# Performance work log

Measured on AMD Instinct MI355X. Metric: run time of the kernel, lower is better.

Reference implementation:

```python
import jax, jax.numpy as jnp
import numpy as np

LSTM_H = 4

def spp(x):
    # x: (N, C, H, W) -> (N, C*5) via adaptive max pool at levels [2, 1]
    N, C, H, W = x.shape
    p2 = x.reshape(N, C, 2, H // 2, 2, W // 2).max(axis=(3, 5)).reshape(N, C * 4)
    p1 = x.max(axis=(2, 3))  # (N, C)
    return jnp.concatenate([p2, p1], axis=1)  # (N, 15)

def setup_inputs() -> dict:
    key = jax.random.key(0)
    ks = jax.random.split(key, 12)
    B, S, C, H, W = 16, 128, 3, 224, 224
    s = 0.1
    return {
        "frames": jax.random.normal(ks[0], (B, S, C, H, W), dtype=jnp.float32),
        "Wf": jax.random.normal(ks[1], (15, 15), dtype=jnp.float32) * s,
        "bf": jax.random.normal(ks[2], (15,), dtype=jnp.float32) * s,
        "We": jax.random.normal(ks[3], (8, 15), dtype=jnp.float32) * s,
        "be": jax.random.normal(ks[4], (8,), dtype=jnp.float32) * s,
        "Wih": jax.random.normal(ks[5], (4 * LSTM_H, 8), dtype=jnp.float32) * s,
        "Whh": jax.random.normal(ks[6], (4 * LSTM_H, LSTM_H), dtype=jnp.float32) * s,
        "bih": jax.random.normal(ks[7], (4 * LSTM_H,), dtype=jnp.float32) * s,
        "bhh": jax.random.normal(ks[8], (4 * LSTM_H,), dtype=jnp.float32) * s,
        "Wp": jax.random.normal(ks[9], (1, LSTM_H), dtype=jnp.float32) * s,
        "bp": jax.random.normal(ks[10], (1,), dtype=jnp.float32) * s,
    }

def _lstm_cell(x, h, c, Wih, Whh, bih, bhh):
    gates = x @ Wih.T + h @ Whh.T + bih + bhh  # (B, 4H)
    i, f, g, o = jnp.split(gates, 4, axis=-1)  # torch gate order: i, f, g, o
    c2 = jax.nn.sigmoid(f) * c + jax.nn.sigmoid(i) * jnp.tanh(g)
    h2 = jax.nn.sigmoid(o) * jnp.tanh(c2)
    return h2, c2

def reference(frames, Wf, bf, We, be, Wih, Whh, bih, bhh, Wp, bp):
    B, S, C, H, W = frames.shape
    pooled_flat = spp(frames.reshape(B * S, C, H, W))          # (B*S, 15)
    forecasted_flat = pooled_flat @ Wf.T + bf                   # (B*S, 15)
    pooled = pooled_flat.reshape(B, S, 15)
    forecasted_pooled = forecasted_flat.reshape(B, S, 15)

    emb = pooled @ We.T + be                 # (B, S, 8)
    femb = forecasted_pooled @ We.T + be     # (B, S, 8)

    def step(carry, xs):
        h, c = carry
        e_t, fe_t = xs                       # each (B, 8)
        h1, c1 = _lstm_cell(e_t, h, c, Wih, Whh, bih, bhh)
        h2, _ = _lstm_cell(fe_t, h1, c1, Wih, Whh, bih, bhh)
        return (h1, c1), (h1, h2)

    h0 = jnp.zeros((B, LSTM_H), dtype=frames.dtype)
    c0 = jnp.zeros((B, LSTM_H), dtype=frames.dtype)
    xs = (jnp.swapaxes(emb, 0, 1), jnp.swapaxes(femb, 0, 1))   # (S, B, 8)
    _, (hs, fhs) = jax.lax.scan(step, (h0, c0), xs)            # (S, B, 4)

    progress = jax.nn.sigmoid(hs @ Wp.T + bp)[..., 0].T        # (B, S)
    forecasted_progress = jax.nn.sigmoid(fhs @ Wp.T + bp)[..., 0].T
    return (progress, forecasted_progress, pooled, forecasted_pooled)
```

## Files before the change

kernel.cpp:

```cpp
#include <hip/hip_runtime.h>
#include <math.h>

#define NEGINF (-INFINITY)

__global__ __launch_bounds__(256) void spp_kernel(const float* __restrict__ frames,
                                                  float* __restrict__ quad) {
    int cimg = blockIdx.x;
    const float4* __restrict__ base =
        reinterpret_cast<const float4*>(frames) + (size_t)cimg * 12544;
    int tid = threadIdx.x;
    float tl = NEGINF, tr = NEGINF, bl = NEGINF, br = NEGINF;
#pragma unroll 7
    for (int it = 0; it < 49; ++it) {
        int idx = (it << 8) + tid;
        float4 f = base[idx];
        float m = fmaxf(fmaxf(f.x, f.y), fmaxf(f.z, f.w));
        int row = idx / 56;
        int c4  = idx - row * 56;
        bool top  = row < 112;
        bool left = c4 < 28;
        float mt = top ? m : NEGINF;
        float mb = top ? NEGINF : m;
        tl = fmaxf(tl, left ? mt : NEGINF);
        tr = fmaxf(tr, left ? NEGINF : mt);
        bl = fmaxf(bl, left ? mb : NEGINF);
        br = fmaxf(br, left ? NEGINF : mb);
    }
#pragma unroll
    for (int m = 32; m >= 1; m >>= 1) {
        tl = fmaxf(tl, __shfl_xor(tl, m, 64));
        tr = fmaxf(tr, __shfl_xor(tr, m, 64));
        bl = fmaxf(bl, __shfl_xor(bl, m, 64));
        br = fmaxf(br, __shfl_xor(br, m, 64));
    }
    __shared__ float s[4][4];
    int w = tid >> 6;
    if ((tid & 63) == 0) { s[w][0] = tl; s[w][1] = tr; s[w][2] = bl; s[w][3] = br; }
    __syncthreads();
    if (tid < 4) {
        float r = fmaxf(fmaxf(s[0][tid], s[1][tid]), fmaxf(s[2][tid], s[3][tid]));
        quad[cimg * 4 + tid] = r;
    }
}

#define BSTRIDE 1036

template <int M>
__device__ __forceinline__ float qbcast(float v) {
    return __int_as_float(
        __builtin_amdgcn_update_dpp(0, __float_as_int(v), M * 0x55, 0xF, 0xF, true));
}

__device__ __forceinline__ float fsigmoid(float z) { return 1.f / (1.f + __expf(-z)); }
__device__ __forceinline__ float ftanh(float z) {
    z = fminf(fmaxf(z, -20.f), 20.f);
    float e = __expf(2.f * z);
    return (e - 1.f) / (e + 1.f);
}

__device__ __forceinline__ float dot8(const float4& a, const float4& b,
                                      const float* __restrict__ w) {
    return a.x * w[0] + a.y * w[1] + a.z * w[2] + a.w * w[3] +
           b.x * w[4] + b.y * w[5] + b.z * w[6] + b.w * w[7];
}

__global__ __launch_bounds__(512, 1) void prep_lstm_kernel(
    const float* __restrict__ quad, const float* __restrict__ Wf,
    const float* __restrict__ bf, const float* __restrict__ We,
    const float* __restrict__ be, const float* __restrict__ Wih,
    const float* __restrict__ Whh, const float* __restrict__ bih,
    const float* __restrict__ bhh, const float* __restrict__ Wp,
    const float* __restrict__ bp, float* __restrict__ out_pooled,
    float* __restrict__ out_fc, float* __restrict__ prog,
    float* __restrict__ fprog) {
    extern __shared__ float lds[];
    float* lemb  = lds;
    float* lfemb = lds + 16 * BSTRIDE;
    int tid = threadIdx.x;

    for (int n = tid; n < 2048; n += 512) {
        float p[15];
        float4 q0 = *(const float4*)(quad + n * 12);
        float4 q1 = *(const float4*)(quad + n * 12 + 4);
        float4 q2 = *(const float4*)(quad + n * 12 + 8);
        p[0] = q0.x; p[1] = q0.y; p[2] = q0.z; p[3] = q0.w;
        p[4] = q1.x; p[5] = q1.y; p[6] = q1.z; p[7] = q1.w;
        p[8] = q2.x; p[9] = q2.y; p[10] = q2.z; p[11] = q2.w;
#pragma unroll
        for (int c = 0; c < 3; c++)
            p[12 + c] = fmaxf(fmaxf(p[c * 4 + 0], p[c * 4 + 1]),
                              fmaxf(p[c * 4 + 2], p[c * 4 + 3]));
#pragma unroll
        for (int j = 0; j < 15; j++) out_pooled[n * 15 + j] = p[j];
        float fc[15];
#pragma unroll
        for (int j = 0; j < 15; j++) {
            float a = bf[j];
#pragma unroll
            for (int kk = 0; kk < 15; kk++) a += p[kk] * Wf[j * 15 + kk];
            fc[j] = a;
            out_fc[n * 15 + j] = a;
        }
        int b = n >> 7, sidx = n & 127;
        float* le = lemb  + b * BSTRIDE + sidx * 8;
        float* lf = lfemb + b * BSTRIDE + sidx * 8;
#pragma unroll
        for (int j = 0; j < 8; j++) {
            float a = be[j], a2 = be[j];
#pragma unroll
            for (int kk = 0; kk < 15; kk++) {
                a  += p[kk]  * We[j * 15 + kk];
                a2 += fc[kk] * We[j * 15 + kk];
            }
            le[j] = a;
            lf[j] = a2;
        }
    }
    __syncthreads();

    if (tid >= 64) return;
    int b = tid >> 2, k = tid & 3;
    float wih[4][8], whh[4][4], bsum[4];
#pragma unroll
    for (int g = 0; g < 4; g++) {
        int row = g * 4 + k;
#pragma unroll
        for (int m = 0; m < 8; m++) wih[g][m] = Wih[row * 8 + m];
#pragma unroll
        for (int m = 0; m < 4; m++) whh[g][m] = Whh[row * 4 + m];
        bsum[g] = bih[row] + bhh[row];
    }
    float wpv[4];
#pragma unroll
    for (int m = 0; m < 4; m++) wpv[m] = Wp[m];
    float bpv = bp[0];

    const float* xe = lemb  + b * BSTRIDE;
    const float* xf = lfemb + b * BSTRIDE;

    float xd1[4], xd2[4];
    {
        float4 a0 = *(const float4*)(xe);
        float4 a1 = *(const float4*)(xe + 4);
        float4 f0 = *(const float4*)(xf);
        float4 f1 = *(const float4*)(xf + 4);
#pragma unroll
        for (int g = 0; g < 4; g++) {
            xd1[g] = bsum[g] + dot8(a0, a1, wih[g]);
            xd2[g] = bsum[g] + dot8(f0, f1, wih[g]);
        }
    }

    float h0 = 0.f, h1r = 0.f, h2r = 0.f, h3r = 0.f;
    float ck = 0.f;

    for (int s2 = 0; s2 < 128; ++s2) {
        const float* nxe = xe + (s2 + 1) * 8;
        const float* nxf = xf + (s2 + 1) * 8;
        float4 na0 = *(const float4*)(nxe);
        float4 na1 = *(const float4*)(nxe + 4);
        float4 nf0 = *(const float4*)(nxf);
        float4 nf1 = *(const float4*)(nxf + 4);

        float g0 = xd1[0] + h0 * whh[0][0] + h1r * whh[0][1] + h2r * whh[0][2] + h3r * whh[0][3];
        float g1 = xd1[1] + h0 * whh[1][0] + h1r * whh[1][1] + h2r * whh[1][2] + h3r * whh[1][3];
        float g2 = xd1[2] + h0 * whh[2][0] + h1r * whh[2][1] + h2r * whh[2][2] + h3r * whh[2][3];
        float g3 = xd1[3] + h0 * whh[3][0] + h1r * whh[3][1] + h2r * whh[3][2] + h3r * whh[3][3];
        float c1  = fsigmoid(g1) * ck + fsigmoid(g0) * ftanh(g2);
        float hk1 = fsigmoid(g3) * ftanh(c1);
        float b0 = qbcast<0>(hk1), b1 = qbcast<1>(hk1), b2 = qbcast<2>(hk1), b3 = qbcast<3>(hk1);
        float z = bpv + b0 * wpv[0] + b1 * wpv[1] + b2 * wpv[2] + b3 * wpv[3];
        if (k == 0) prog[b * 128 + s2] = fsigmoid(z);

        float e0 = xd2[0] + b0 * whh[0][0] + b1 * whh[0][1] + b2 * whh[0][2] + b3 * whh[0][3];
        float e1 = xd2[1] + b0 * whh[1][0] + b1 * whh[1][1] + b2 * whh[1][2] + b3 * whh[1][3];
        float e2 = xd2[2] + b0 * whh[2][0] + b1 * whh[2][1] + b2 * whh[2][2] + b3 * whh[2][3];
        float e3 = xd2[3] + b0 * whh[3][0] + b1 * whh[3][1] + b2 * whh[3][2] + b3 * whh[3][3];
        float c2v = fsigmoid(e1) * c1 + fsigmoid(e0) * ftanh(e2);
        float hk2 = fsigmoid(e3) * ftanh(c2v);
        float d0 = qbcast<0>(hk2), d1 = qbcast<1>(hk2), d2 = qbcast<2>(hk2), d3 = qbcast<3>(hk2);
        float z2 = bpv + d0 * wpv[0] + d1 * wpv[1] + d2 * wpv[2] + d3 * wpv[3];
        if (k == 0) fprog[b * 128 + s2] = fsigmoid(z2);

        h0 = b0; h1r = b1; h2r = b2; h3r = b3; ck = c1;

#pragma unroll
        for (int g = 0; g < 4; g++) {
            xd1[g] = bsum[g] + dot8(na0, na1, wih[g]);
            xd2[g] = bsum[g] + dot8(nf0, nf1, wih[g]);
        }
    }
}

extern "C" void kernel_launch(void* const* d_in, const int* in_sizes, int n_in,
                              void* d_out, int out_size, void* d_ws, size_t ws_size,
                              hipStream_t stream) {
    const float* frames = (const float*)d_in[0];
    const float* Wf     = (const float*)d_in[1];
    const float* bf     = (const float*)d_in[2];
    const float* We     = (const float*)d_in[3];
    const float* be     = (const float*)d_in[4];
    const float* Wih    = (const float*)d_in[5];
    const float* Whh    = (const float*)d_in[6];
    const float* bih    = (const float*)d_in[7];
    const float* bhh    = (const float*)d_in[8];
    const float* Wp     = (const float*)d_in[9];
    const float* bp     = (const float*)d_in[10];

    float* out = (float*)d_out;
    float* out_prog   = out;
    float* out_fprog  = out + 2048;
    float* out_pooled = out + 4096;
    float* out_fc     = out + 4096 + 30720;

    float* quad = (float*)d_ws;

    spp_kernel<<<6144, 256, 0, stream>>>(frames, quad);
    size_t lds_bytes = (size_t)2 * 16 * BSTRIDE * sizeof(float);
    prep_lstm_kernel<<<1, 512, lds_bytes, stream>>>(quad, Wf, bf, We, be, Wih, Whh,
                                                    bih, bhh, Wp, bp, out_pooled,
                                                    out_fc, out_prog, out_fprog);
}
```

Before: 310.7 us.

## Fuse SPP and LSTM into one persistent kernel with per-timestep flag sync

The pooling kernel and the single-block prep/LSTM kernel become one launch of 257 blocks. Block 0 runs the LSTM recurrence and waits on per-timestep atomic counters, while 256 producer blocks pool frames in timestep order and write the embeddings to global memory. This lets the serial LSTM overlap the memory-bound pooling and removes the separate serial prep pass. In exchange, producers drop from 6144 blocks to 256, each handling a whole 3-channel image at a time. The design also relies on all blocks being co-resident to avoid deadlock, and it adds a memset launch.

```diff
diff --git a/kernel.cpp b/kernel.cpp
--- a/kernel.cpp
+++ b/kernel.cpp
@@ -2,55 +2,13 @@
 #include <math.h>
 
 #define NEGINF (-INFINITY)
-
-__global__ __launch_bounds__(256) void spp_kernel(const float* __restrict__ frames,
-                                                  float* __restrict__ quad) {
-    int cimg = blockIdx.x;
-    const float4* __restrict__ base =
-        reinterpret_cast<const float4*>(frames) + (size_t)cimg * 12544;
-    int tid = threadIdx.x;
-    float tl = NEGINF, tr = NEGINF, bl = NEGINF, br = NEGINF;
-#pragma unroll 7
-    for (int it = 0; it < 49; ++it) {
-        int idx = (it << 8) + tid;
-        float4 f = base[idx];
-        float m = fmaxf(fmaxf(f.x, f.y), fmaxf(f.z, f.w));
-        int row = idx / 56;
-        int c4  = idx - row * 56;
-        bool top  = row < 112;
-        bool left = c4 < 28;
-        float mt = top ? m : NEGINF;
-        float mb = top ? NEGINF : m;
-        tl = fmaxf(tl, left ? mt : NEGINF);
-        tr = fmaxf(tr, left ? NEGINF : mt);
-        bl = fmaxf(bl, left ? mb : NEGINF);
-        br = fmaxf(br, left ? NEGINF : mb);
-    }
-#pragma unroll
-    for (int m = 32; m >= 1; m >>= 1) {
-        tl = fmaxf(tl, __shfl_xor(tl, m, 64));
-        tr = fmaxf(tr, __shfl_xor(tr, m, 64));
-        bl = fmaxf(bl, __shfl_xor(bl, m, 64));
-        br = fmaxf(br, __shfl_xor(br, m, 64));
-    }
-    __shared__ float s[4][4];
-    int w = tid >> 6;
-    if ((tid & 63) == 0) { s[w][0] = tl; s[w][1] = tr; s[w][2] = bl; s[w][3] = br; }
-    __syncthreads();
-    if (tid < 4) {
-        float r = fmaxf(fmaxf(s[0][tid], s[1][tid]), fmaxf(s[2][tid], s[3][tid]));
-        quad[cimg * 4 + tid] = r;
-    }
-}
-
-#define BSTRIDE 1036
+#define AGENT __HIP_MEMORY_SCOPE_AGENT
 
 template <int M>
 __device__ __forceinline__ float qbcast(float v) {
     return __int_as_float(
         __builtin_amdgcn_update_dpp(0, __float_as_int(v), M * 0x55, 0xF, 0xF, true));
 }
-
 __device__ __forceinline__ float fsigmoid(float z) { return 1.f / (1.f + __expf(-z)); }
 __device__ __forceinline__ float ftanh(float z) {
     z = fminf(fmaxf(z, -20.f), 20.f);
@@ -58,65 +16,100 @@
     return (e - 1.f) / (e + 1.f);
 }
 
-__device__ __forceinline__ float dot8(const float4& a, const float4& b,
-                                      const float* __restrict__ w) {
-    return a.x * w[0] + a.y * w[1] + a.z * w[2] + a.w * w[3] +
-           b.x * w[4] + b.y * w[5] + b.z * w[6] + b.w * w[7];
-}
-
-__global__ __launch_bounds__(512, 1) void prep_lstm_kernel(
-    const float* __restrict__ quad, const float* __restrict__ Wf,
+__global__ __launch_bounds__(256) void fused_kernel(
+    const float* __restrict__ frames, const float* __restrict__ Wf,
     const float* __restrict__ bf, const float* __restrict__ We,
     const float* __restrict__ be, const float* __restrict__ Wih,
     const float* __restrict__ Whh, const float* __restrict__ bih,
     const float* __restrict__ bhh, const float* __restrict__ Wp,
     const float* __restrict__ bp, float* __restrict__ out_pooled,
     float* __restrict__ out_fc, float* __restrict__ prog,
-    float* __restrict__ fprog) {
-    extern __shared__ float lds[];
-    float* lemb  = lds;
-    float* lfemb = lds + 16 * BSTRIDE;
+    float* __restrict__ fprog, float* __restrict__ emb,
+    float* __restrict__ femb, int* __restrict__ cnt) {
     int tid = threadIdx.x;
 
-    for (int n = tid; n < 2048; n += 512) {
-        float p[15];
-        float4 q0 = *(const float4*)(quad + n * 12);
-        float4 q1 = *(const float4*)(quad + n * 12 + 4);
-        float4 q2 = *(const float4*)(quad + n * 12 + 8);
-        p[0] = q0.x; p[1] = q0.y; p[2] = q0.z; p[3] = q0.w;
-        p[4] = q1.x; p[5] = q1.y; p[6] = q1.z; p[7] = q1.w;
-        p[8] = q2.x; p[9] = q2.y; p[10] = q2.z; p[11] = q2.w;
-#pragma unroll
-        for (int c = 0; c < 3; c++)
-            p[12 + c] = fmaxf(fmaxf(p[c * 4 + 0], p[c * 4 + 1]),
-                              fmaxf(p[c * 4 + 2], p[c * 4 + 3]));
-#pragma unroll
-        for (int j = 0; j < 15; j++) out_pooled[n * 15 + j] = p[j];
-        float fc[15];
-#pragma unroll
-        for (int j = 0; j < 15; j++) {
-            float a = bf[j];
-#pragma unroll
-            for (int kk = 0; kk < 15; kk++) a += p[kk] * Wf[j * 15 + kk];
-            fc[j] = a;
-            out_fc[n * 15 + j] = a;
+    if (blockIdx.x > 0) {
+        int pid = blockIdx.x - 1;
+        __shared__ float sw[4][4];
+        __shared__ float sq[3][4];
+        __shared__ float sp[15];
+        __shared__ float sfc[15];
+        for (int r = 0; r < 8; ++r) {
+            int nidx = r * 256 + pid;
+            int s = nidx >> 4, b = nidx & 15;
+            int n = b * 128 + s;
+            const float4* __restrict__ base =
+                reinterpret_cast<const float4*>(frames) + (size_t)n * 37632;
+            for (int c = 0; c < 3; ++c) {
+                const float4* __restrict__ pb = base + c * 12544;
+                float tl = NEGINF, tr = NEGINF, bl = NEGINF, br = NEGINF;
+#pragma unroll 7
+                for (int it = 0; it < 49; ++it) {
+                    int i2 = (it << 8) + tid;
+                    float4 f = pb[i2];
+                    float m = fmaxf(fmaxf(f.x, f.y), fmaxf(f.z, f.w));
+                    int row = i2 / 56;
+                    int c4 = i2 - row * 56;
+                    bool top = row < 112;
+                    bool left = c4 < 28;
+                    float mt = top ? m : NEGINF;
+                    float mb = top ? NEGINF : m;
+                    tl = fmaxf(tl, left ? mt : NEGINF);
+                    tr = fmaxf(tr, left ? NEGINF : mt);
+                    bl = fmaxf(bl, left ? mb : NEGINF);
+                    br = fmaxf(br, left ? NEGINF : mb);
+                }
+#pragma unroll
+                for (int m = 32; m >= 1; m >>= 1) {
+                    tl = fmaxf(tl, __shfl_xor(tl, m, 64));
+                    tr = fmaxf(tr, __shfl_xor(tr, m, 64));
+                    bl = fmaxf(bl, __shfl_xor(bl, m, 64));
+                    br = fmaxf(br, __shfl_xor(br, m, 64));
+                }
+                int w = tid >> 6;
+                if ((tid & 63) == 0) { sw[w][0] = tl; sw[w][1] = tr; sw[w][2] = bl; sw[w][3] = br; }
+                __syncthreads();
+                if (tid < 4)
+                    sq[c][tid] = fmaxf(fmaxf(sw[0][tid], sw[1][tid]),
+                                       fmaxf(sw[2][tid], sw[3][tid]));
+                __syncthreads();
+            }
+            if (tid == 0) {
+#pragma unroll
+                for (int c = 0; c < 3; ++c) {
+                    float a = sq[c][0], bq = sq[c][1], cq = sq[c][2], d = sq[c][3];
+                    sp[c * 4 + 0] = a; sp[c * 4 + 1] = bq;
+                    sp[c * 4 + 2] = cq; sp[c * 4 + 3] = d;
+                    sp[12 + c] = fmaxf(fmaxf(a, bq), fmaxf(cq, d));
+                }
+            }
+            __syncthreads();
+            if (tid < 15) {
+                float a = bf[tid];
+#pragma unroll
+                for (int kk = 0; kk < 15; ++kk) a += sp[kk] * Wf[tid * 15 + kk];
+                sfc[tid] = a;
+                out_pooled[n * 15 + tid] = sp[tid];
+                out_fc[n * 15 + tid] = a;
+            }
+            __syncthreads();
+            if (tid < 8) {
+                float a = be[tid], a2 = be[tid];
+#pragma unroll
+                for (int kk = 0; kk < 15; ++kk) {
+                    a += sp[kk] * We[tid * 15 + kk];
+                    a2 += sfc[kk] * We[tid * 15 + kk];
+                }
+                __hip_atomic_store(&emb[n * 8 + tid], a, __ATOMIC_RELAXED, AGENT);
+                __hip_atomic_store(&femb[n * 8 + tid], a2, __ATOMIC_RELAXED, AGENT);
+            }
+            __syncthreads();
+            if (tid == 0)
+                __hip_atomic_fetch_add(&cnt[s], 1, __ATOMIC_RELEASE, AGENT);
+            __syncthreads();
         }
-        int b = n >> 7, sidx = n & 127;
-        float* le = lemb  + b * BSTRIDE + sidx * 8;
-        float* lf = lfemb + b * BSTRIDE + sidx * 8;
-#pragma unroll
-        for (int j = 0; j < 8; j++) {
-            float a = be[j], a2 = be[j];
-#pragma unroll
-            for (int kk = 0; kk < 15; kk++) {
-                a  += p[kk]  * We[j * 15 + kk];
-                a2 += fc[kk] * We[j * 15 + kk];
-            }
-            le[j] = a;
-            lf[j] = a2;
-        }
+        return;
     }
-    __syncthreads();
 
     if (tid >= 64) return;
     int b = tid >> 2, k = tid & 3;
@@ -135,42 +128,43 @@
     for (int m = 0; m < 4; m++) wpv[m] = Wp[m];
     float bpv = bp[0];
 
-    const float* xe = lemb  + b * BSTRIDE;
-    const float* xf = lfemb + b * BSTRIDE;
-
-    float xd1[4], xd2[4];
-    {
-        float4 a0 = *(const float4*)(xe);
-        float4 a1 = *(const float4*)(xe + 4);
-        float4 f0 = *(const float4*)(xf);
-        float4 f1 = *(const float4*)(xf + 4);
-#pragma unroll
-        for (int g = 0; g < 4; g++) {
-            xd1[g] = bsum[g] + dot8(a0, a1, wih[g]);
-            xd2[g] = bsum[g] + dot8(f0, f1, wih[g]);
-        }
-    }
-
     float h0 = 0.f, h1r = 0.f, h2r = 0.f, h3r = 0.f;
     float ck = 0.f;
 
-    for (int s2 = 0; s2 < 128; ++s2) {
-        const float* nxe = xe + (s2 + 1) * 8;
-        const float* nxf = xf + (s2 + 1) * 8;
-        float4 na0 = *(const float4*)(nxe);
-        float4 na1 = *(const float4*)(nxe + 4);
-        float4 nf0 = *(const float4*)(nxf);
-        float4 nf1 = *(const float4*)(nxf + 4);
+    for (int s = 0; s < 128; ++s) {
+        while (__hip_atomic_load(&cnt[s], __ATOMIC_ACQUIRE, AGENT) < 16) {
+            __builtin_amdgcn_s_sleep(1);
+        }
+        float* xe = emb + (size_t)(b * 128 + s) * 8;
+        float* xf = femb + (size_t)(b * 128 + s) * 8;
+        float x1[8], x2[8];
+#pragma unroll
+        for (int m = 0; m < 8; m++) x1[m] = __hip_atomic_load(&xe[m], __ATOMIC_RELAXED, AGENT);
+#pragma unroll
+        for (int m = 0; m < 8; m++) x2[m] = __hip_atomic_load(&xf[m], __ATOMIC_RELAXED, AGENT);
+
+        float xd1[4], xd2[4];
+#pragma unroll
+        for (int g = 0; g < 4; g++) {
+            float a = bsum[g], a2 = bsum[g];
+#pragma unroll
+            for (int m = 0; m < 8; m++) {
+                a += x1[m] * wih[g][m];
+                a2 += x2[m] * wih[g][m];
+            }
+            xd1[g] = a;
+            xd2[g] = a2;
+        }
 
         float g0 = xd1[0] + h0 * whh[0][0] + h1r * whh[0][1] + h2r * whh[0][2] + h3r * whh[0][3];
         float g1 = xd1[1] + h0 * whh[1][0] + h1r * whh[1][1] + h2r * whh[1][2] + h3r * whh[1][3];
         float g2 = xd1[2] + h0 * whh[2][0] + h1r * whh[2][1] + h2r * whh[2][2] + h3r * whh[2][3];
         float g3 = xd1[3] + h0 * whh[3][0] + h1r * whh[3][1] + h2r * whh[3][2] + h3r * whh[3][3];
-        float c1  = fsigmoid(g1) * ck + fsigmoid(g0) * ftanh(g2);
+        float c1 = fsigmoid(g1) * ck + fsigmoid(g0) * ftanh(g2);
         float hk1 = fsigmoid(g3) * ftanh(c1);
         float b0 = qbcast<0>(hk1), b1 = qbcast<1>(hk1), b2 = qbcast<2>(hk1), b3 = qbcast<3>(hk1);
         float z = bpv + b0 * wpv[0] + b1 * wpv[1] + b2 * wpv[2] + b3 * wpv[3];
-        if (k == 0) prog[b * 128 + s2] = fsigmoid(z);
+        if (k == 0) prog[b * 128 + s] = fsigmoid(z);
 
         float e0 = xd2[0] + b0 * whh[0][0] + b1 * whh[0][1] + b2 * whh[0][2] + b3 * whh[0][3];
         float e1 = xd2[1] + b0 * whh[1][0] + b1 * whh[1][1] + b2 * whh[1][2] + b3 * whh[1][3];
@@ -180,15 +174,9 @@
         float hk2 = fsigmoid(e3) * ftanh(c2v);
         float d0 = qbcast<0>(hk2), d1 = qbcast<1>(hk2), d2 = qbcast<2>(hk2), d3 = qbcast<3>(hk2);
         float z2 = bpv + d0 * wpv[0] + d1 * wpv[1] + d2 * wpv[2] + d3 * wpv[3];
-        if (k == 0) fprog[b * 128 + s2] = fsigmoid(z2);
+        if (k == 0) fprog[b * 128 + s] = fsigmoid(z2);
 
         h0 = b0; h1r = b1; h2r = b2; h3r = b3; ck = c1;
-
-#pragma unroll
-        for (int g = 0; g < 4; g++) {
-            xd1[g] = bsum[g] + dot8(na0, na1, wih[g]);
-            xd2[g] = bsum[g] + dot8(nf0, nf1, wih[g]);
-        }
     }
 }
 
@@ -213,11 +201,13 @@
     float* out_pooled = out + 4096;
     float* out_fc     = out + 4096 + 30720;
 
-    float* quad = (float*)d_ws;
-
-    spp_kernel<<<6144, 256, 0, stream>>>(frames, quad);
-    size_t lds_bytes = (size_t)2 * 16 * BSTRIDE * sizeof(float);
-    prep_lstm_kernel<<<1, 512, lds_bytes, stream>>>(quad, Wf, bf, We, be, Wih, Whh,
-                                                    bih, bhh, Wp, bp, out_pooled,
-                                                    out_fc, out_prog, out_fprog);
-}
+    char* ws = (char*)d_ws;
+    int*   cnt  = (int*)ws;
+    float* emb  = (float*)(ws + 512);
+    float* femb = (float*)(ws + 512 + 65536);
+
+    hipMemsetAsync(cnt, 0, 128 * sizeof(int), stream);
+    fused_kernel<<<257, 256, 0, stream>>>(frames, Wf, bf, We, be, Wih, Whh, bih,
+                                          bhh, Wp, bp, out_pooled, out_fc,
+                                          out_prog, out_fprog, emb, femb, cnt);
+}
```

New measurement: 344.2 us. 1.11x slower.
